# Kernel tuning notes

Hardware: AMD Instinct MI355X
Metric: run time of the kernel (lower is better)

The kernel has to match this reference:

```python
import jax, jax.numpy as jnp
import numpy as np

B, E, DIM = 8, 2048, 512
KERNEL = 8
DECAY_CONSTANT = 1.0


def _forward(x, weight, bias, decay_value):
    # x: (B, E, S) with S == dim; weight: (K, S); bias: (S,); decay_value: (2, 1)
    K, dim = weight.shape
    Bb, Ee, S = x.shape
    i = jnp.arange(dim)[:, None]
    j = jnp.arange(dim)[None, :]
    # decayed upper-triangular weight: W[k, i, j] = weight[k, j] * dv^((j-i)/c) for j >= i
    dv = jnp.clip(decay_value[1, 0], 0.9, 1.0)
    d = dv ** ((j - i).astype(x.dtype) / DECAY_CONSTANT)  # (S, S)
    W = jnp.where(j >= i, weight[:, None, :] * d[None], jnp.zeros((), x.dtype))  # (K, S, S)
    p = K - 1
    padded = jnp.pad(x, ((0, 0), (p, p), (0, 0)))  # zero-pad sequence axis
    # shifted stack: stacked[b, k, e] = x[b, e + k - (K-1)] (zeros out of range) -> causal taps
    stacked = jnp.stack([padded[:, k:Ee + k] for k in range(K)], axis=1)  # (B, K, E, S)
    out = jnp.einsum('bkei,kij->bej', stacked, W) + bias
    return out


def setup_inputs() -> dict:
    key = jax.random.key(0)
    k1, k2 = jax.random.split(key)
    x = jax.random.normal(k1, (B, E, DIM), dtype=jnp.float32)
    weight = jax.random.normal(k2, (KERNEL, DIM), dtype=jnp.float32)
    bias = jnp.zeros((DIM,), dtype=jnp.float32)
    decay_value = jnp.ones((2, 1), dtype=jnp.float32)
    return {"x": x, "weight": weight, "bias": bias, "decay_value": decay_value}


def reference(x, weight, bias, decay_value):
    return _forward(x, weight, bias, decay_value)
```

## Files before the change

kernel.cpp:

```cpp
#include <hip/hip_runtime.h>


#define B_    8
#define E_    2048
#define DIM_  512
#define K_    8
#define TE    32
#define STRIP 64
#define HALO  (K_ - 1)
#define NRA   (TE + HALO)
#define NRB   TE
#define LSTR  516
#define NF4A  (NRA * 128)
#define NF4B  (NRB * 128)

typedef __attribute__((address_space(1))) const float gfloat_t;
typedef __attribute__((address_space(3))) float       sfloat_t;

__device__ __forceinline__ void gld16(float* lds, const float* g)
{
    __builtin_amdgcn_global_load_lds((gfloat_t*)g, (sfloat_t*)lds, 16, 0, 0);
}

__device__ __forceinline__ void scan_rows(float* __restrict__ yls, int rowbase,
    int nrows, int t, float d1, float d2, float d3, float d4,
    float d128, float d256)
{
    const int lane = t & 63, wave = t >> 6;
    const int r16 = lane & 15, seg = lane >> 4;
    const int rw  = wave * 16 + r16;
    if (rw >= nrows) return;
    float* sp = &yls[(rowbase + rw) * LSTR + seg * 128];

    float E = 0.f;
    #pragma unroll 8
    for (int q = 0; q < 32; ++q) {
        const float4 v = *(const float4*)(sp + 4 * q);
        const float p = fmaf(d3, v.x, fmaf(d2, v.y, fmaf(d1, v.z, v.w)));
        E = fmaf(d4, E, p);
    }
    float S = E;
    float u1 = __shfl_up(S, 16, 64); if (seg >= 1) S = fmaf(d128, u1, S);
    float u2 = __shfl_up(S, 32, 64); if (seg >= 2) S = fmaf(d256, u2, S);
    float C  = __shfl_up(S, 16, 64); if (seg == 0) C = 0.f;
    float prev = C;
    #pragma unroll 8
    for (int q = 0; q < 32; ++q) {
        const float4 v = *(const float4*)(sp + 4 * q);
        const float p01   = fmaf(d1, v.x, v.y);
        const float p012  = fmaf(d1, p01, v.z);
        const float p0123 = fmaf(d1, p012, v.w);
        float4 yv;
        yv.x = fmaf(d1, prev, v.x);
        yv.y = fmaf(d2, prev, p01);
        yv.z = fmaf(d3, prev, p012);
        yv.w = fmaf(d4, prev, p0123);
        prev = yv.w;
        *(float4*)(sp + 4 * q) = yv;
    }
}

__device__ __forceinline__ void conv8(const float* __restrict__ yls,
    float* __restrict__ out, int b, int e0, int o0, int jf,
    const float4 (&w)[K_], float4 bi)
{
    float4 win[K_];
    #pragma unroll
    for (int k = 0; k < 7; ++k)
        win[k] = *(const float4*)(&yls[(o0 + k) * LSTR + jf]);
    #pragma unroll
    for (int i = 0; i < 8; ++i) {
        const int o = o0 + i;
        win[7] = *(const float4*)(&yls[(o + 7) * LSTR + jf]);
        float4 acc = bi;
        #pragma unroll
        for (int k = 0; k < K_; ++k) {
            acc.x = fmaf(w[k].x, win[k].x, acc.x);
            acc.y = fmaf(w[k].y, win[k].y, acc.y);
            acc.z = fmaf(w[k].z, win[k].z, acc.z);
            acc.w = fmaf(w[k].w, win[k].w, acc.w);
        }
        *(float4*)(out + ((size_t)b * E_ + e0 + o) * DIM_ + jf) = acc;
        #pragma unroll
        for (int k = 0; k < 7; ++k) win[k] = win[k + 1];
    }
}

__global__ __launch_bounds__(512) void krl_p(
    const float* __restrict__ x,
    const float* __restrict__ weight,
    const float* __restrict__ bias,
    const float* __restrict__ decay,
    float* __restrict__ out)
{
    __shared__ float yls[(NRA + NRB) * LSTR];

    const int t  = threadIdx.x;
    const int b  = blockIdx.y;
    const int e0 = blockIdx.x * STRIP;
    const int ebase = e0 - HALO;
    const float* xb = x + (size_t)b * E_ * DIM_;

    const int j = t & 127, h = t >> 7;
    const int jf = j * 4;
    float4 w[K_];
    #pragma unroll
    for (int k = 0; k < K_; ++k) w[k] = *(const float4*)(weight + k * DIM_ + jf);
    const float4 bi = *(const float4*)(bias + jf);

    float dv = decay[1];
    dv = fminf(fmaxf(dv, 0.9f), 1.0f);
    const float d1 = dv, d2 = dv * dv, d3 = d2 * dv, d4 = d2 * d2;
    float d128 = d4;
    d128 *= d128; d128 *= d128; d128 *= d128; d128 *= d128; d128 *= d128;
    const float d256 = d128 * d128;

    for (int i = t; i < NF4A; i += 512) {
        const int r = i >> 7, f4 = i & 127;
        const int eg = ebase + r;
        float* lp = &yls[r * LSTR + f4 * 4];
        if (eg >= 0) gld16(lp, xb + (size_t)eg * DIM_ + f4 * 4);
        else         *(float4*)lp = make_float4(0.f, 0.f, 0.f, 0.f);
    }
    __syncthreads();

    for (int i = t; i < NF4B; i += 512) {
        const int r = i >> 7, f4 = i & 127;
        gld16(&yls[(NRA + r) * LSTR + f4 * 4],
              xb + (size_t)(e0 + TE + r) * DIM_ + f4 * 4);
    }

    scan_rows(yls, 0, NRA, t, d1, d2, d3, d4, d128, d256);

    asm volatile("s_waitcnt lgkmcnt(0)\n\ts_barrier" ::: "memory");

    conv8(yls, out, b, e0, h * 8, jf, w, bi);

    asm volatile("s_waitcnt vmcnt(8)\n\ts_barrier" ::: "memory");

    scan_rows(yls, NRA, NRB, t, d1, d2, d3, d4, d128, d256);

    asm volatile("s_waitcnt lgkmcnt(0)\n\ts_barrier" ::: "memory");

    conv8(yls, out, b, e0, 32 + h * 8, jf, w, bi);
}

extern "C" void kernel_launch(void* const* d_in, const int* in_sizes, int n_in,
                              void* d_out, int out_size, void* d_ws, size_t ws_size,
                              hipStream_t stream) {
    const float* x      = (const float*)d_in[0];
    const float* weight = (const float*)d_in[1];
    const float* bias   = (const float*)d_in[2];
    const float* decay  = (const float*)d_in[3];
    float* out = (float*)d_out;

    dim3 grid(E_ / STRIP, B_);
    dim3 block(512);
    krl_p<<<grid, block, 0, stream>>>(x, weight, bias, decay, out);
}
```

Before: 90.96 us.

## Replace two-phase pipelined strip with single-tile block per 32 rows

Each block now handles one 32-row tile plus its 7-row halo rather than a 64-row strip split into two phases. The in-block overlap of the second tile's async global-to-LDS load with the first tile's scan and convolution is removed, and the custom waitcnt barriers become plain syncthreads. This doubles the grid and shrinks LDS use per block, which may let more blocks share a CU. The cost is that halo rows are loaded and scanned once per 32 rows instead of once per 64.

```diff
diff --git a/kernel.cpp b/kernel.cpp
--- a/kernel.cpp
+++ b/kernel.cpp
@@ -6,13 +6,10 @@
 #define DIM_  512
 #define K_    8
 #define TE    32
-#define STRIP 64
 #define HALO  (K_ - 1)
-#define NRA   (TE + HALO)
-#define NRB   TE
+#define NROWS (TE + HALO)
 #define LSTR  516
-#define NF4A  (NRA * 128)
-#define NF4B  (NRB * 128)
+#define NF4   (NROWS * 128)
 
 typedef __attribute__((address_space(1))) const float gfloat_t;
 typedef __attribute__((address_space(3))) float       sfloat_t;
@@ -22,82 +19,18 @@
     __builtin_amdgcn_global_load_lds((gfloat_t*)g, (sfloat_t*)lds, 16, 0, 0);
 }
 
-__device__ __forceinline__ void scan_rows(float* __restrict__ yls, int rowbase,
-    int nrows, int t, float d1, float d2, float d3, float d4,
-    float d128, float d256)
-{
-    const int lane = t & 63, wave = t >> 6;
-    const int r16 = lane & 15, seg = lane >> 4;
-    const int rw  = wave * 16 + r16;
-    if (rw >= nrows) return;
-    float* sp = &yls[(rowbase + rw) * LSTR + seg * 128];
-
-    float E = 0.f;
-    #pragma unroll 8
-    for (int q = 0; q < 32; ++q) {
-        const float4 v = *(const float4*)(sp + 4 * q);
-        const float p = fmaf(d3, v.x, fmaf(d2, v.y, fmaf(d1, v.z, v.w)));
-        E = fmaf(d4, E, p);
-    }
-    float S = E;
-    float u1 = __shfl_up(S, 16, 64); if (seg >= 1) S = fmaf(d128, u1, S);
-    float u2 = __shfl_up(S, 32, 64); if (seg >= 2) S = fmaf(d256, u2, S);
-    float C  = __shfl_up(S, 16, 64); if (seg == 0) C = 0.f;
-    float prev = C;
-    #pragma unroll 8
-    for (int q = 0; q < 32; ++q) {
-        const float4 v = *(const float4*)(sp + 4 * q);
-        const float p01   = fmaf(d1, v.x, v.y);
-        const float p012  = fmaf(d1, p01, v.z);
-        const float p0123 = fmaf(d1, p012, v.w);
-        float4 yv;
-        yv.x = fmaf(d1, prev, v.x);
-        yv.y = fmaf(d2, prev, p01);
-        yv.z = fmaf(d3, prev, p012);
-        yv.w = fmaf(d4, prev, p0123);
-        prev = yv.w;
-        *(float4*)(sp + 4 * q) = yv;
-    }
-}
-
-__device__ __forceinline__ void conv8(const float* __restrict__ yls,
-    float* __restrict__ out, int b, int e0, int o0, int jf,
-    const float4 (&w)[K_], float4 bi)
-{
-    float4 win[K_];
-    #pragma unroll
-    for (int k = 0; k < 7; ++k)
-        win[k] = *(const float4*)(&yls[(o0 + k) * LSTR + jf]);
-    #pragma unroll
-    for (int i = 0; i < 8; ++i) {
-        const int o = o0 + i;
-        win[7] = *(const float4*)(&yls[(o + 7) * LSTR + jf]);
-        float4 acc = bi;
-        #pragma unroll
-        for (int k = 0; k < K_; ++k) {
-            acc.x = fmaf(w[k].x, win[k].x, acc.x);
-            acc.y = fmaf(w[k].y, win[k].y, acc.y);
-            acc.z = fmaf(w[k].z, win[k].z, acc.z);
-            acc.w = fmaf(w[k].w, win[k].w, acc.w);
-        }
-        *(float4*)(out + ((size_t)b * E_ + e0 + o) * DIM_ + jf) = acc;
-        #pragma unroll
-        for (int k = 0; k < 7; ++k) win[k] = win[k + 1];
-    }
-}
-
-__global__ __launch_bounds__(512) void krl_p(
+__global__ __launch_bounds__(512) void krl_w(
     const float* __restrict__ x,
     const float* __restrict__ weight,
     const float* __restrict__ bias,
     const float* __restrict__ decay,
     float* __restrict__ out)
 {
-    __shared__ float yls[(NRA + NRB) * LSTR];
+    __shared__ float yls[NROWS * LSTR];
 
     const int t  = threadIdx.x;
     const int b  = blockIdx.y;
-    const int e0 = blockIdx.x * STRIP;
+    const int e0 = blockIdx.x * TE;
     const int ebase = e0 - HALO;
     const float* xb = x + (size_t)b * E_ * DIM_;
 
@@ -115,7 +48,7 @@
     d128 *= d128; d128 *= d128; d128 *= d128; d128 *= d128; d128 *= d128;
     const float d256 = d128 * d128;
 
-    for (int i = t; i < NF4A; i += 512) {
+    for (int i = t; i < NF4; i += 512) {
         const int r = i >> 7, f4 = i & 127;
         const int eg = ebase + r;
         float* lp = &yls[r * LSTR + f4 * 4];
@@ -124,25 +57,66 @@
     }
     __syncthreads();
 
-    for (int i = t; i < NF4B; i += 512) {
-        const int r = i >> 7, f4 = i & 127;
-        gld16(&yls[(NRA + r) * LSTR + f4 * 4],
-              xb + (size_t)(e0 + TE + r) * DIM_ + f4 * 4);
+    {
+        const int lane = t & 63, wave = t >> 6;
+        const int r16 = lane & 15, seg = lane >> 4;
+        const int row = wave * 16 + r16;
+        if (row < NROWS) {
+            float* sp = &yls[row * LSTR + seg * 128];
+
+            float E = 0.f;
+            #pragma unroll 8
+            for (int q = 0; q < 32; ++q) {
+                const float4 v = *(const float4*)(sp + 4 * q);
+                const float p = fmaf(d3, v.x, fmaf(d2, v.y, fmaf(d1, v.z, v.w)));
+                E = fmaf(d4, E, p);
+            }
+            float S = E;
+            float u1 = __shfl_up(S, 16, 64); if (seg >= 1) S = fmaf(d128, u1, S);
+            float u2 = __shfl_up(S, 32, 64); if (seg >= 2) S = fmaf(d256, u2, S);
+            float C  = __shfl_up(S, 16, 64); if (seg == 0) C = 0.f;
+            float prev = C;
+            #pragma unroll 8
+            for (int q = 0; q < 32; ++q) {
+                const float4 v = *(const float4*)(sp + 4 * q);
+                const float p01   = fmaf(d1, v.x, v.y);
+                const float p012  = fmaf(d1, p01, v.z);
+                const float p0123 = fmaf(d1, p012, v.w);
+                float4 yv;
+                yv.x = fmaf(d1, prev, v.x);
+                yv.y = fmaf(d2, prev, p01);
+                yv.z = fmaf(d3, prev, p012);
+                yv.w = fmaf(d4, prev, p0123);
+                prev = yv.w;
+                *(float4*)(sp + 4 * q) = yv;
+            }
+        }
     }
+    __syncthreads();
 
-    scan_rows(yls, 0, NRA, t, d1, d2, d3, d4, d128, d256);
-
-    asm volatile("s_waitcnt lgkmcnt(0)\n\ts_barrier" ::: "memory");
-
-    conv8(yls, out, b, e0, h * 8, jf, w, bi);
-
-    asm volatile("s_waitcnt vmcnt(8)\n\ts_barrier" ::: "memory");
-
-    scan_rows(yls, NRA, NRB, t, d1, d2, d3, d4, d128, d256);
-
-    asm volatile("s_waitcnt lgkmcnt(0)\n\ts_barrier" ::: "memory");
-
-    conv8(yls, out, b, e0, 32 + h * 8, jf, w, bi);
+    {
+        const int o0 = h * 8;
+        float4 win[K_];
+        #pragma unroll
+        for (int k = 0; k < 7; ++k)
+            win[k] = *(const float4*)(&yls[(o0 + k) * LSTR + jf]);
+        #pragma unroll
+        for (int i = 0; i < 8; ++i) {
+            const int o = o0 + i;
+            win[7] = *(const float4*)(&yls[(o + 7) * LSTR + jf]);
+            float4 acc = bi;
+            #pragma unroll
+            for (int k = 0; k < K_; ++k) {
+                acc.x = fmaf(w[k].x, win[k].x, acc.x);
+                acc.y = fmaf(w[k].y, win[k].y, acc.y);
+                acc.z = fmaf(w[k].z, win[k].z, acc.z);
+                acc.w = fmaf(w[k].w, win[k].w, acc.w);
+            }
+            *(float4*)(out + ((size_t)b * E_ + e0 + o) * DIM_ + jf) = acc;
+            #pragma unroll
+            for (int k = 0; k < 7; ++k) win[k] = win[k + 1];
+        }
+    }
 }
 
 extern "C" void kernel_launch(void* const* d_in, const int* in_sizes, int n_in,
@@ -154,7 +128,7 @@
     const float* decay  = (const float*)d_in[3];
     float* out = (float*)d_out;
 
-    dim3 grid(E_ / STRIP, B_);
+    dim3 grid(E_ / TE, B_);
     dim3 block(512);
-    krl_p<<<grid, block, 0, stream>>>(x, weight, bias, decay, out);
+    krl_w<<<grid, block, 0, stream>>>(x, weight, bias, decay, out);
 }
```

New measurement: 89.93 us. Within noise of the previous version (-1.1%).
